# Performance work log

Measured on AMD Instinct MI355X. Metric: run time of the kernel, lower is better.

## Reference

```python
import jax, jax.numpy as jnp
import numpy as np


def setup_inputs() -> dict:
    key = jax.random.key(0)
    k1, k2 = jax.random.split(key)
    B, L, D, R = 32, 512, 1024, 128
    batch = jax.random.normal(k1, (B, L, D), dtype=jnp.float32)
    # nn.init.uniform_(proj, -0.05, 0.05)
    proj = jax.random.uniform(k2, (D, R), dtype=jnp.float32, minval=-0.05, maxval=0.05)
    return {"batch": batch, "proj": proj}


def reference(batch, proj):
    # transformed: (B, L, R)
    t = jnp.matmul(batch, proj)
    # Squared L2 all-pairs distance via ||a||^2 + ||b||^2 - 2 a.b
    # (same math as sum((t_i - t_j)^2, -1), avoids the O(B*L*L*R) intermediate)
    sq_norms = jnp.sum(t * t, axis=-1)                      # (B, L)
    cross = jnp.einsum("bir,bjr->bij", t, t)               # (B, L, L)
    d = sq_norms[:, :, None] + sq_norms[:, None, :] - 2.0 * cross
    return jnp.maximum(d, 0.0)  # clamp tiny negative numerical noise
```

## Files before the change

### kernel.cpp

```cpp
#include <hip/hip_runtime.h>
#include <hip/hip_bf16.h>


typedef __attribute__((ext_vector_type(8))) short bf16x8;
typedef __attribute__((ext_vector_type(4))) float f32x4;

__device__ __forceinline__ unsigned short f2bf(float f) {
    unsigned u = __float_as_uint(f);
    unsigned r = (u + 0x7fffu + ((u >> 16) & 1u)) >> 16;
    return (unsigned short)r;
}
__device__ __forceinline__ float bf2f(unsigned short h) {
    return __uint_as_float(((unsigned)h) << 16);
}
__device__ __forceinline__ bf16x8 pack8(float4 x, float4 y) {
    bf16x8 r;
    r[0] = (short)f2bf(x.x); r[1] = (short)f2bf(x.y);
    r[2] = (short)f2bf(x.z); r[3] = (short)f2bf(x.w);
    r[4] = (short)f2bf(y.x); r[5] = (short)f2bf(y.y);
    r[6] = (short)f2bf(y.z); r[7] = (short)f2bf(y.w);
    return r;
}

__global__ __launch_bounds__(256) void transpose_proj(const float* __restrict__ proj,
                                                      unsigned short* __restrict__ projT) {
    __shared__ unsigned short TsT[128][40];
    const int k0 = blockIdx.x * 32;
    const int t = threadIdx.x;
    const int kl = t >> 3;
    const int seg = t & 7;
    const float* src = proj + (k0 + kl) * 128 + seg * 16;
#pragma unroll
    for (int i = 0; i < 4; ++i) {
        float4 v = *(const float4*)(src + 4 * i);
        int c = seg * 16 + 4 * i;
        TsT[c + 0][kl] = f2bf(v.x);
        TsT[c + 1][kl] = f2bf(v.y);
        TsT[c + 2][kl] = f2bf(v.z);
        TsT[c + 3][kl] = f2bf(v.w);
    }
    __syncthreads();
    const int r = t >> 1, h = t & 1;
#pragma unroll
    for (int i = 0; i < 2; ++i) {
        *(uint4*)(projT + r * 1024 + k0 + h * 16 + 8 * i) =
            *(const uint4*)&TsT[r][h * 16 + 8 * i];
    }
}

__global__ __launch_bounds__(256) void gemm_t(const float* __restrict__ batch,
                                              const unsigned short* __restrict__ projT,
                                              unsigned short* __restrict__ tOut,
                                              float* __restrict__ sqn) {
    __shared__ unsigned short Bs[128][72];
    __shared__ float sqpart[2][2][16];

    const int t = threadIdx.x;
    const int wave = t >> 6, lane = t & 63;
    const int wm = wave >> 1, wn = wave & 1;
    const int quad = lane >> 4, l15 = lane & 15;
    const int m0 = blockIdx.x * 32;

    f32x4 acc[4] = {};

    const float* aptr = batch + (m0 + wm * 16 + l15) * 1024 + quad * 8;
    const int br = t >> 1, bh = t & 1;
    const uint4* bsrc0 = (const uint4*)(projT + br * 1024 + bh * 32);

    for (int kk = 0; kk < 1024; kk += 64) {
        const uint4* bsrc = (const uint4*)((const unsigned short*)bsrc0 + kk);
        uint4 b0 = bsrc[0], b1 = bsrc[1], b2 = bsrc[2], b3 = bsrc[3];
        float4 a0 = *(const float4*)(aptr + kk);
        float4 a1 = *(const float4*)(aptr + kk + 4);
        float4 a2 = *(const float4*)(aptr + kk + 32);
        float4 a3 = *(const float4*)(aptr + kk + 36);
        __syncthreads();
        *(uint4*)&Bs[br][bh * 32 + 0]  = b0;
        *(uint4*)&Bs[br][bh * 32 + 8]  = b1;
        *(uint4*)&Bs[br][bh * 32 + 16] = b2;
        *(uint4*)&Bs[br][bh * 32 + 24] = b3;
        __syncthreads();

        bf16x8 af0 = pack8(a0, a1);
        bf16x8 af1 = pack8(a2, a3);
#pragma unroll
        for (int fn = 0; fn < 4; ++fn) {
            bf16x8 bf_ = *(const bf16x8*)&Bs[wn * 64 + fn * 16 + l15][quad * 8];
            acc[fn] = __builtin_amdgcn_mfma_f32_16x16x32_bf16(af0, bf_, acc[fn], 0, 0, 0);
        }
#pragma unroll
        for (int fn = 0; fn < 4; ++fn) {
            bf16x8 bf_ = *(const bf16x8*)&Bs[wn * 64 + fn * 16 + l15][32 + quad * 8];
            acc[fn] = __builtin_amdgcn_mfma_f32_16x16x32_bf16(af1, bf_, acc[fn], 0, 0, 0);
        }
    }

    float p[4] = {0.f, 0.f, 0.f, 0.f};
#pragma unroll
    for (int fn = 0; fn < 4; ++fn) {
        int col = wn * 64 + fn * 16 + l15;
#pragma unroll
        for (int reg = 0; reg < 4; ++reg) {
            int row = m0 + wm * 16 + quad * 4 + reg;
            unsigned short hb = f2bf(acc[fn][reg]);
            tOut[row * 128 + col] = hb;
            float fv = bf2f(hb);
            p[reg] += fv * fv;
        }
    }
#pragma unroll
    for (int off = 1; off < 16; off <<= 1) {
#pragma unroll
        for (int reg = 0; reg < 4; ++reg) p[reg] += __shfl_xor(p[reg], off);
    }
    if (l15 == 0) {
#pragma unroll
        for (int reg = 0; reg < 4; ++reg) sqpart[wm][wn][quad * 4 + reg] = p[reg];
    }
    __syncthreads();
    if (t < 32) {
        int wmi = t >> 4, ridx = t & 15;
        sqn[m0 + wmi * 16 + ridx] = sqpart[wmi][0][ridx] + sqpart[wmi][1][ridx];
    }
}

__global__ __launch_bounds__(256) void dist_k(const unsigned short* __restrict__ tMat,
                                              const float* __restrict__ sqn,
                                              float* __restrict__ out) {
    __shared__ unsigned short Tj[128][136];
    __shared__ float sqis[128], sqjs[128];

    const int bx = blockIdx.x;
    const int b = bx >> 4, it = (bx >> 2) & 3, jt = bx & 3;
    const int i0 = it * 128, j0 = jt * 128;
    const int t = threadIdx.x;
    const int wave = t >> 6, lane = t & 63;
    const int quad = lane >> 4, l15 = lane & 15;

    const unsigned short* abase = tMat + (b * 512 + i0 + wave * 32 + l15) * 128 + quad * 8;
    uint4 araw[2][4];
#pragma unroll
    for (int fm = 0; fm < 2; ++fm)
#pragma unroll
        for (int ksi = 0; ksi < 4; ++ksi)
            araw[fm][ksi] = *(const uint4*)(abase + fm * 16 * 128 + ksi * 32);

    {
        const int r = t >> 1, h = t & 1;
        const uint4* jsrc = (const uint4*)(tMat + (b * 512 + j0 + r) * 128 + h * 64);
#pragma unroll
        for (int i = 0; i < 8; ++i)
            *(uint4*)&Tj[r][h * 64 + 8 * i] = jsrc[i];
    }
    if (t < 128) sqis[t] = sqn[b * 512 + i0 + t];
    else         sqjs[t - 128] = sqn[b * 512 + j0 + (t - 128)];
    __syncthreads();

    f32x4 acc[2][8] = {};
#pragma unroll
    for (int ksi = 0; ksi < 4; ++ksi) {
        bf16x8 bfr[8];
#pragma unroll
        for (int fn = 0; fn < 8; ++fn)
            bfr[fn] = *(const bf16x8*)&Tj[fn * 16 + l15][ksi * 32 + quad * 8];
#pragma unroll
        for (int fm = 0; fm < 2; ++fm) {
            bf16x8 af = *(const bf16x8*)&araw[fm][ksi];
#pragma unroll
            for (int fn = 0; fn < 8; ++fn)
                acc[fm][fn] = __builtin_amdgcn_mfma_f32_16x16x32_bf16(af, bfr[fn], acc[fm][fn], 0, 0, 0);
        }
    }

    float* obase = out + (size_t)b * 512 * 512;
#pragma unroll
    for (int fm = 0; fm < 2; ++fm) {
#pragma unroll
        for (int reg = 0; reg < 4; ++reg) {
            int il = wave * 32 + fm * 16 + quad * 4 + reg;
            float si = sqis[il];
#pragma unroll
            for (int fn = 0; fn < 8; ++fn) {
                int jl = fn * 16 + l15;
                float v = si + sqjs[jl] - 2.0f * acc[fm][fn][reg];
                obase[(size_t)(i0 + il) * 512 + (j0 + jl)] = fmaxf(v, 0.0f);
            }
        }
    }
}

extern "C" void kernel_launch(void* const* d_in, const int* in_sizes, int n_in,
                              void* d_out, int out_size, void* d_ws, size_t ws_size,
                              hipStream_t stream) {
    (void)in_sizes; (void)n_in; (void)out_size; (void)ws_size;
    const float* batch = (const float*)d_in[0];
    const float* proj  = (const float*)d_in[1];
    float* out = (float*)d_out;

    unsigned short* projT = (unsigned short*)d_ws;
    unsigned short* tMat  = projT + 128 * 1024;
    float* sqn = (float*)(tMat + 16384 * 128);

    hipLaunchKernelGGL(transpose_proj, dim3(32),  dim3(256), 0, stream, proj, projT);
    hipLaunchKernelGGL(gemm_t,         dim3(512), dim3(256), 0, stream, batch, projT, tMat, sqn);
    hipLaunchKernelGGL(dist_k,         dim3(512), dim3(256), 0, stream, tMat, sqn, out);
}
```

Before: 128.9 us.

## Drop LDS staging in both GEMMs and store distance tiles with float4 writes

The projection GEMM now loads B fragments directly from global memory (L2-resident projT) into registers, removing the LDS tile and both block barriers per k-step, and unrolls the k loop by two. The distance kernel swaps the roles of the i and j tiles so each lane's accumulator registers map to four consecutive output columns, which allows 16-byte vectorized stores instead of scalar ones. It also drops the shared Tj tile and the squared-norm arrays, reading fragments and norms straight from global memory. The trade-off is redundant global and L2 fragment reads across waves in exchange for no LDS traffic, no barriers, and wider output writes.

```diff
diff --git a/kernel.cpp b/kernel.cpp
--- a/kernel.cpp
+++ b/kernel.cpp
@@ -52,7 +52,6 @@
                                               const unsigned short* __restrict__ projT,
                                               unsigned short* __restrict__ tOut,
                                               float* __restrict__ sqn) {
-    __shared__ unsigned short Bs[128][72];
     __shared__ float sqpart[2][2][16];
 
     const int t = threadIdx.x;
@@ -64,35 +63,31 @@
     f32x4 acc[4] = {};
 
     const float* aptr = batch + (m0 + wm * 16 + l15) * 1024 + quad * 8;
-    const int br = t >> 1, bh = t & 1;
-    const uint4* bsrc0 = (const uint4*)(projT + br * 1024 + bh * 32);
-
+    const unsigned short* bptr[4];
+#pragma unroll
+    for (int fn = 0; fn < 4; ++fn)
+        bptr[fn] = projT + (wn * 64 + fn * 16 + l15) * 1024 + quad * 8;
+
+#pragma unroll 2
     for (int kk = 0; kk < 1024; kk += 64) {
-        const uint4* bsrc = (const uint4*)((const unsigned short*)bsrc0 + kk);
-        uint4 b0 = bsrc[0], b1 = bsrc[1], b2 = bsrc[2], b3 = bsrc[3];
         float4 a0 = *(const float4*)(aptr + kk);
         float4 a1 = *(const float4*)(aptr + kk + 4);
         float4 a2 = *(const float4*)(aptr + kk + 32);
         float4 a3 = *(const float4*)(aptr + kk + 36);
-        __syncthreads();
-        *(uint4*)&Bs[br][bh * 32 + 0]  = b0;
-        *(uint4*)&Bs[br][bh * 32 + 8]  = b1;
-        *(uint4*)&Bs[br][bh * 32 + 16] = b2;
-        *(uint4*)&Bs[br][bh * 32 + 24] = b3;
-        __syncthreads();
-
+        bf16x8 b0[4], b1[4];
+#pragma unroll
+        for (int fn = 0; fn < 4; ++fn) {
+            b0[fn] = *(const bf16x8*)(bptr[fn] + kk);
+            b1[fn] = *(const bf16x8*)(bptr[fn] + kk + 32);
+        }
         bf16x8 af0 = pack8(a0, a1);
         bf16x8 af1 = pack8(a2, a3);
 #pragma unroll
-        for (int fn = 0; fn < 4; ++fn) {
-            bf16x8 bf_ = *(const bf16x8*)&Bs[wn * 64 + fn * 16 + l15][quad * 8];
-            acc[fn] = __builtin_amdgcn_mfma_f32_16x16x32_bf16(af0, bf_, acc[fn], 0, 0, 0);
-        }
-#pragma unroll
-        for (int fn = 0; fn < 4; ++fn) {
-            bf16x8 bf_ = *(const bf16x8*)&Bs[wn * 64 + fn * 16 + l15][32 + quad * 8];
-            acc[fn] = __builtin_amdgcn_mfma_f32_16x16x32_bf16(af1, bf_, acc[fn], 0, 0, 0);
-        }
+        for (int fn = 0; fn < 4; ++fn)
+            acc[fn] = __builtin_amdgcn_mfma_f32_16x16x32_bf16(af0, b0[fn], acc[fn], 0, 0, 0);
+#pragma unroll
+        for (int fn = 0; fn < 4; ++fn)
+            acc[fn] = __builtin_amdgcn_mfma_f32_16x16x32_bf16(af1, b1[fn], acc[fn], 0, 0, 0);
     }
 
     float p[4] = {0.f, 0.f, 0.f, 0.f};
@@ -127,9 +122,6 @@
 __global__ __launch_bounds__(256) void dist_k(const unsigned short* __restrict__ tMat,
                                               const float* __restrict__ sqn,
                                               float* __restrict__ out) {
-    __shared__ unsigned short Tj[128][136];
-    __shared__ float sqis[128], sqjs[128];
-
     const int bx = blockIdx.x;
     const int b = bx >> 4, it = (bx >> 2) & 3, jt = bx & 3;
     const int i0 = it * 128, j0 = jt * 128;
@@ -137,7 +129,7 @@
     const int wave = t >> 6, lane = t & 63;
     const int quad = lane >> 4, l15 = lane & 15;
 
-    const unsigned short* abase = tMat + (b * 512 + i0 + wave * 32 + l15) * 128 + quad * 8;
+    const unsigned short* abase = tMat + (b * 512 + j0 + wave * 32 + l15) * 128 + quad * 8;
     uint4 araw[2][4];
 #pragma unroll
     for (int fm = 0; fm < 2; ++fm)
@@ -145,16 +137,18 @@
         for (int ksi = 0; ksi < 4; ++ksi)
             araw[fm][ksi] = *(const uint4*)(abase + fm * 16 * 128 + ksi * 32);
 
-    {
-        const int r = t >> 1, h = t & 1;
-        const uint4* jsrc = (const uint4*)(tMat + (b * 512 + j0 + r) * 128 + h * 64);
-#pragma unroll
-        for (int i = 0; i < 8; ++i)
-            *(uint4*)&Tj[r][h * 64 + 8 * i] = jsrc[i];
-    }
-    if (t < 128) sqis[t] = sqn[b * 512 + i0 + t];
-    else         sqjs[t - 128] = sqn[b * 512 + j0 + (t - 128)];
-    __syncthreads();
+    const float* sqb = sqn + b * 512;
+    float sqj_[2][4], sqi_[8];
+#pragma unroll
+    for (int fm = 0; fm < 2; ++fm)
+#pragma unroll
+        for (int reg = 0; reg < 4; ++reg)
+            sqj_[fm][reg] = sqb[j0 + wave * 32 + fm * 16 + quad * 4 + reg];
+#pragma unroll
+    for (int fn = 0; fn < 8; ++fn)
+        sqi_[fn] = sqb[i0 + fn * 16 + l15];
+
+    const unsigned short* bbase = tMat + (b * 512 + i0 + l15) * 128 + quad * 8;
 
     f32x4 acc[2][8] = {};
 #pragma unroll
@@ -162,7 +156,7 @@
         bf16x8 bfr[8];
 #pragma unroll
         for (int fn = 0; fn < 8; ++fn)
-            bfr[fn] = *(const bf16x8*)&Tj[fn * 16 + l15][ksi * 32 + quad * 8];
+            bfr[fn] = *(const bf16x8*)(bbase + fn * 16 * 128 + ksi * 32);
 #pragma unroll
         for (int fm = 0; fm < 2; ++fm) {
             bf16x8 af = *(const bf16x8*)&araw[fm][ksi];
@@ -174,17 +168,18 @@
 
     float* obase = out + (size_t)b * 512 * 512;
 #pragma unroll
-    for (int fm = 0; fm < 2; ++fm) {
-#pragma unroll
-        for (int reg = 0; reg < 4; ++reg) {
-            int il = wave * 32 + fm * 16 + quad * 4 + reg;
-            float si = sqis[il];
-#pragma unroll
-            for (int fn = 0; fn < 8; ++fn) {
-                int jl = fn * 16 + l15;
-                float v = si + sqjs[jl] - 2.0f * acc[fm][fn][reg];
-                obase[(size_t)(i0 + il) * 512 + (j0 + jl)] = fmaxf(v, 0.0f);
-            }
+    for (int fn = 0; fn < 8; ++fn) {
+        const int i = i0 + fn * 16 + l15;
+        float* orow = obase + (size_t)i * 512 + j0;
+        const float si = sqi_[fn];
+#pragma unroll
+        for (int fm = 0; fm < 2; ++fm) {
+            float4 v;
+            v.x = fmaxf(si + sqj_[fm][0] - 2.0f * acc[fm][fn][0], 0.0f);
+            v.y = fmaxf(si + sqj_[fm][1] - 2.0f * acc[fm][fn][1], 0.0f);
+            v.z = fmaxf(si + sqj_[fm][2] - 2.0f * acc[fm][fn][2], 0.0f);
+            v.w = fmaxf(si + sqj_[fm][3] - 2.0f * acc[fm][fn][3], 0.0f);
+            *(float4*)(orow + wave * 32 + fm * 16 + quad * 4) = v;
         }
     }
 }
```

Measured after the change: 148.5 us. 1.15x slower.
